# Optimization experiments

Measured on AMD Instinct MI355X. Metric: run time of the kernel, lower is better.

## Reference

```python
import jax, jax.numpy as jnp
import numpy as np

B, C, H, W = 16, 512, 32, 32
NH = 8
HD = C // NH


def setup_inputs() -> dict:
    key = jax.random.key(0)
    k1, k2, k3 = jax.random.split(key, 3)
    x = jax.random.normal(k1, (B, C, H, W), dtype=jnp.float32)
    w_qkv = jax.random.normal(k2, (3 * C, C), dtype=jnp.float32) * (1.0 / np.sqrt(C))
    w_proj = jax.random.normal(k3, (C, C), dtype=jnp.float32) * (1.0 / np.sqrt(C))
    b_proj = jnp.zeros((C,), dtype=jnp.float32)
    return {"x": x, "w_qkv": w_qkv, "w_proj": w_proj, "b_proj": b_proj}


def reference(x, w_qkv, w_proj, b_proj):
    b, c, h, w = x.shape
    n = h * w
    # 1x1 conv qkv: (3C, C) applied per pixel
    qkv = jnp.einsum('oc,bchw->bohw', w_qkv, x)  # [B, 3C, H, W]
    qkv = qkv.reshape(b, 3, NH, HD, n)           # [B, 3, nh, hd, N]
    qkv = jnp.transpose(qkv, (1, 0, 2, 4, 3))    # [3, B, nh, N, hd]
    q, k, v = qkv[0], qkv[1], qkv[2]
    scale = HD ** -0.5
    scores = jnp.einsum('bhnd,bhmd->bhnm', q, k) * scale  # [B, nh, N, N]
    attn = jax.nn.softmax(scores, axis=-1)
    out = jnp.einsum('bhnm,bhmd->bhnd', attn, v)          # [B, nh, N, hd]
    out = jnp.transpose(out, (0, 1, 3, 2)).reshape(b, c, h, w)
    # 1x1 conv proj with bias
    out = jnp.einsum('oc,bchw->bohw', w_proj, out) + b_proj[None, :, None, None]
    return out
```

## Files before the change

### kernel.cpp

```cpp
#include <hip/hip_runtime.h>
#include <hip/hip_bf16.h>
#include <math.h>

#define BB 16
#define CC 512
#define NH 8
#define HD 64
#define NN 1024
#define THREEC 1536

#define QSCALE 0.18033688f

typedef __attribute__((ext_vector_type(8))) short bf16x8;
typedef __attribute__((ext_vector_type(4))) float f32x4;
typedef __attribute__((ext_vector_type(16))) float f32x16;

#if __has_builtin(__builtin_amdgcn_exp2f)
#define EXP2F __builtin_amdgcn_exp2f
#else
#define EXP2F exp2f
#endif

#define XT_OFF 0u
#define WQ_OFF 16777216u
#define WP_OFF 18350080u
#define QB_OFF 18874368u
#define KB_OFF 35651584u
#define VT_OFF 52428800u
#define AB_OFF 69206016u

static __device__ inline unsigned short f2bf(float f) {
  union { float f; unsigned u; } v; v.f = f;
  unsigned r = v.u + 0x7fffu + ((v.u >> 16) & 1u);
  return (unsigned short)(r >> 16);
}

static __device__ inline unsigned pk2bf(float a, float b) {
#if defined(__AMDGCN__) && __has_builtin(__builtin_amdgcn_cvt_pk_bf16_f32)
  typedef __attribute__((ext_vector_type(2))) __bf16 bfp2;
  union { bfp2 v; unsigned u; } z;
  z.v = __builtin_amdgcn_cvt_pk_bf16_f32(a, b);
  return z.u;
#else
  return (unsigned)f2bf(a) | ((unsigned)f2bf(b) << 16);
#endif
}

static __device__ inline void gld_lds16(const unsigned short* g, unsigned short* l) {
  __builtin_amdgcn_global_load_lds(
      (const __attribute__((address_space(1))) unsigned int*)g,
      (__attribute__((address_space(3))) unsigned int*)l, 16, 0, 0);
}

__global__ __launch_bounds__(256) void prep_w(const float* __restrict__ wqkv,
                                              const float* __restrict__ wproj,
                                              unsigned short* __restrict__ dq,
                                              unsigned short* __restrict__ dp) {
  const size_t i8 = ((size_t)blockIdx.x * 256 + threadIdx.x) * 8;
  const float* src;
  unsigned short* dst;
  if (i8 < 786432u) { src = wqkv + i8; dst = dq + i8; }
  else              { src = wproj + (i8 - 786432u); dst = dp + (i8 - 786432u); }
  float4 a = *(const float4*)src;
  float4 b = *(const float4*)(src + 4);
  unsigned short pk[8] = {f2bf(a.x), f2bf(a.y), f2bf(a.z), f2bf(a.w),
                          f2bf(b.x), f2bf(b.y), f2bf(b.z), f2bf(b.w)};
  *(uint4*)dst = *(const uint4*)pk;
}

__global__ __launch_bounds__(256) void prep_xT(const float* __restrict__ x,
                                               unsigned short* __restrict__ xT) {
  const int b  = blockIdx.z;
  const int c0 = blockIdx.y * 64;
  const int n0 = blockIdx.x * 64;
  __shared__ float tile[64][65];
  const int t  = threadIdx.x;
  const int cl = t >> 4, n4 = (t & 15) * 4;
#pragma unroll
  for (int r = 0; r < 4; ++r) {
    float4 v = *(const float4*)&x[((size_t)b * CC + c0 + cl + 16 * r) * NN + n0 + n4];
    *(float4*)&tile[cl + 16 * r][n4] = v;
  }
  __syncthreads();
  const int nl = t >> 4, c4 = (t & 15) * 4;
#pragma unroll
  for (int r = 0; r < 4; ++r) {
    ushort4 p;
    p.x = f2bf(tile[c4 + 0][nl + 16 * r]);
    p.y = f2bf(tile[c4 + 1][nl + 16 * r]);
    p.z = f2bf(tile[c4 + 2][nl + 16 * r]);
    p.w = f2bf(tile[c4 + 3][nl + 16 * r]);
    *(ushort4*)&xT[((size_t)b * NN + n0 + nl + 16 * r) * CC + c0 + c4] = p;
  }
}

__global__ __launch_bounds__(256) void qkv_mfma(const unsigned short* __restrict__ wq,
                                                const unsigned short* __restrict__ xT,
                                                unsigned short* __restrict__ qb,
                                                unsigned short* __restrict__ kb_,
                                                unsigned short* __restrict__ vt) {
  const int b  = blockIdx.z;
  const int o0 = blockIdx.y * 128;
  const int n0 = blockIdx.x * 128;
  const int t  = threadIdx.x;
  const int w    = t >> 6;
  const int lane = t & 63;
  const int quad = lane >> 4;
  const int l16  = lane & 15;
  const int m_off = (w >> 1) * 64;
  const int n_off = (w & 1) * 64;

  __shared__ unsigned short sm[17408];
  unsigned short* As = sm;
  unsigned short* Bs = sm + 8192;

  const int which = o0 >> 9;
  const bool vmode = (which == 2);

  const int srow = lane >> 3;
  const int ssw  = ((lane & 7) ^ srow) * 8;
  const unsigned short* gA = wq + (size_t)(o0 + 32 * w + srow) * CC + ssw;
  const unsigned short* gB = xT + ((size_t)b * NN + n0 + 32 * w + srow) * CC + ssw;

  f32x4 acc[4][4] = {};

  for (int c0 = 0; c0 < CC; c0 += 64) {
    __syncthreads();
#pragma unroll
    for (int L = 0; L < 4; ++L) {
      gld_lds16(gA + (size_t)(8 * L) * CC + c0, &As[(32 * w + 8 * L) * 64]);
      gld_lds16(gB + (size_t)(8 * L) * CC + c0, &Bs[(32 * w + 8 * L) * 64]);
    }
    __syncthreads();
    const unsigned short* Af = vmode ? Bs : As;
    const unsigned short* Bf = vmode ? As : Bs;
#pragma unroll
    for (int ks = 0; ks < 2; ++ks) {
      const int ph = ((ks * 4 + quad) ^ (l16 & 7)) * 8;
      bf16x8 af[4], bfr[4];
#pragma unroll
      for (int i = 0; i < 4; ++i) {
        af[i]  = *(const bf16x8*)&Af[(m_off + 16 * i + l16) * 64 + ph];
        bfr[i] = *(const bf16x8*)&Bf[(n_off + 16 * i + l16) * 64 + ph];
      }
#pragma unroll
      for (int i = 0; i < 4; ++i)
#pragma unroll
        for (int j = 0; j < 4; ++j)
          acc[i][j] = __builtin_amdgcn_mfma_f32_16x16x32_bf16(af[i], bfr[j], acc[i][j], 0, 0, 0);
    }
  }

  __syncthreads();
  const float sc = (which == 0) ? QSCALE : 1.0f;
#pragma unroll
  for (int i = 0; i < 4; ++i) {
#pragma unroll
    for (int j = 0; j < 4; ++j) {
      const int Drow = m_off + 16 * i + quad * 4;
      const int Dcol = n_off + 16 * j + l16;
      ushort4 p;
      p.x = f2bf(acc[i][j][0] * sc);
      p.y = f2bf(acc[i][j][1] * sc);
      p.z = f2bf(acc[i][j][2] * sc);
      p.w = f2bf(acc[i][j][3] * sc);
      *(ushort4*)&sm[Dcol * 136 + Drow] = p;
    }
  }
  __syncthreads();
  const int lrow = t >> 1;
  const int half = t & 1;
  const unsigned short* src = &sm[lrow * 136 + 64 * half];
  if (!vmode) {
    const int hh = ((o0 >> 6) & 7) + half;
    unsigned short* dst = (which == 0 ? qb : kb_) +
        ((size_t)(b * NH + hh) * NN + n0 + lrow) * HD;
#pragma unroll
    for (int i = 0; i < 8; ++i) *(uint4*)(dst + 8 * i) = *(const uint4*)(src + 8 * i);
  } else {
    const int hh = ((o0 + lrow) >> 6) & 7;
    const int d  = lrow & 63;
    unsigned short* dst = vt + ((size_t)(b * NH + hh) * HD + d) * NN + n0 + 64 * half;
#pragma unroll
    for (int i = 0; i < 8; ++i) *(uint4*)(dst + 8 * i) = *(const uint4*)(src + 8 * i);
  }
}

__global__ __launch_bounds__(256) void attn_mfma(const unsigned short* __restrict__ Qg,
                                                 const unsigned short* __restrict__ Kg,
                                                 const unsigned short* __restrict__ Vtg,
                                                 unsigned short* __restrict__ attnB) {
  const int bh = blockIdx.x;
  const int b  = bh >> 3;
  const int h  = bh & 7;
  const int n0 = blockIdx.y * 128;
  const int t  = threadIdx.x;
  const int w    = t >> 6;
  const int lane = t & 63;
  const int l31  = lane & 31;
  const int hi   = lane >> 5;

  __shared__ unsigned short sm[9216];
  unsigned short* Ks = sm;
  unsigned short* Vt = sm + 4096;

  const unsigned short* qrow = Qg + ((size_t)bh * NN + n0 + w * 32 + l31) * HD + hi * 8;
  bf16x8 qf[4];
#pragma unroll
  for (int c = 0; c < 4; ++c) qf[c] = *(const bf16x8*)(qrow + 16 * c);

  const int krow = (l31 & ~12) | ((l31 & 4) << 1) | ((l31 & 8) >> 1);
  const int ksw  = krow & 7;
  const int vsw  = l31 & 7;

  f32x16 oacc[2] = {};
  float lx = 0.f, ly = 0.f;

  const int srow = lane >> 3;
  const int sgrp = (lane & 7) ^ (srow & 7);
  const unsigned short* kstage = Kg + (size_t)bh * NN * HD +
                                 (size_t)(16 * w + srow) * HD + sgrp * 8;
  const unsigned short* vstage = Vtg + (size_t)bh * HD * NN +
                                 (size_t)(16 * w + srow) * NN + sgrp * 8;
  unsigned short* ksl0 = &Ks[(16 * w) * 64];
  unsigned short* ksl1 = &Ks[(16 * w + 8) * 64];
  unsigned short* vsl0 = &Vt[(16 * w) * 64];
  unsigned short* vsl1 = &Vt[(16 * w + 8) * 64];

#pragma unroll 1
  for (int j0 = 0; j0 < NN; j0 += 64) {
    __syncthreads();
    gld_lds16(kstage + (size_t)j0 * HD, ksl0);
    gld_lds16(kstage + (size_t)(j0 + 8) * HD, ksl1);
    gld_lds16(vstage + j0, vsl0);
    gld_lds16(vstage + (size_t)8 * NN + j0, vsl1);
    __syncthreads();

#pragma unroll
    for (int kb = 0; kb < 2; ++kb) {
      f32x16 st = {};
      const unsigned short* krp = &Ks[(32 * kb + krow) * 64];
#pragma unroll
      for (int c = 0; c < 4; ++c) {
        bf16x8 kf = *(const bf16x8*)(krp + (((2 * c + hi) ^ ksw) * 8));
        st = __builtin_amdgcn_mfma_f32_32x32x16_bf16(kf, qf[c], st, 0, 0, 0);
      }
      float e[16];
#pragma unroll
      for (int i = 0; i < 8; ++i) {
        e[2 * i]     = EXP2F(st[2 * i]);
        e[2 * i + 1] = EXP2F(st[2 * i + 1]);
        lx += e[2 * i];
        ly += e[2 * i + 1];
      }
      unsigned P[8];
#pragma unroll
      for (int i = 0; i < 8; ++i) P[i] = pk2bf(e[2 * i], e[2 * i + 1]);

#pragma unroll
      for (int g = 0; g < 2; ++g) {
        union { unsigned u[4]; bf16x8 v; } cv;
        cv.u[0] = P[4 * g + 0]; cv.u[1] = P[4 * g + 1];
        cv.u[2] = P[4 * g + 2]; cv.u[3] = P[4 * g + 3];
#pragma unroll
        for (int mt = 0; mt < 2; ++mt) {
          const int vrow = 32 * mt + l31;
          bf16x8 vf = *(const bf16x8*)&Vt[vrow * 64 + (((4 * kb + 2 * g + hi) ^ vsw) * 8)];
          oacc[mt] = __builtin_amdgcn_mfma_f32_32x32x16_bf16(vf, cv.v, oacc[mt], 0, 0, 0);
        }
      }
    }
  }

  float lsum = lx + ly;
  lsum += __shfl_xor(lsum, 32);
  const float inv = 1.0f / lsum;

  __syncthreads();
  unsigned short* Es = sm + w * 2304;
#pragma unroll
  for (int mt = 0; mt < 2; ++mt) {
#pragma unroll
    for (int rr = 0; rr < 4; ++rr) {
      const int d = 32 * mt + 8 * rr + 4 * hi;
      ushort4 p;
      p.x = f2bf(oacc[mt][4 * rr + 0] * inv);
      p.y = f2bf(oacc[mt][4 * rr + 1] * inv);
      p.z = f2bf(oacc[mt][4 * rr + 2] * inv);
      p.w = f2bf(oacc[mt][4 * rr + 3] * inv);
      *(ushort4*)&Es[l31 * 72 + d] = p;
    }
  }
  const int q    = lane >> 1;
  const int half = lane & 1;
  const unsigned short* src = &Es[q * 72 + 32 * half];
  unsigned short* gdst = attnB + ((size_t)b * NN + n0 + w * 32 + q) * CC + h * HD + 32 * half;
#pragma unroll
  for (int i = 0; i < 4; ++i) *(uint4*)(gdst + 8 * i) = *(const uint4*)(src + 8 * i);
}

__global__ __launch_bounds__(256) void proj_mfma(const unsigned short* __restrict__ wp,
                                                 const unsigned short* __restrict__ aB,
                                                 const float* __restrict__ bias,
                                                 float* __restrict__ out) {
  const int b  = blockIdx.z;
  const int o0 = blockIdx.y * 128;
  const int n0 = blockIdx.x * 128;
  const int t  = threadIdx.x;
  const int w    = t >> 6;
  const int lane = t & 63;
  const int quad = lane >> 4;
  const int l16  = lane & 15;
  const int m_off = (w >> 1) * 64;
  const int n_off = (w & 1) * 64;

  __shared__ unsigned short sm[16384];
  unsigned short* As = sm;
  unsigned short* Bs = sm + 8192;

  const int srow = lane >> 3;
  const int ssw  = ((lane & 7) ^ srow) * 8;
  const unsigned short* gA = wp + (size_t)(o0 + 32 * w + srow) * CC + ssw;
  const unsigned short* gB = aB + ((size_t)b * NN + n0 + 32 * w + srow) * CC + ssw;

  f32x4 acc[4][4] = {};

  for (int c0 = 0; c0 < CC; c0 += 64) {
    __syncthreads();
#pragma unroll
    for (int L = 0; L < 4; ++L) {
      gld_lds16(gA + (size_t)(8 * L) * CC + c0, &As[(32 * w + 8 * L) * 64]);
      gld_lds16(gB + (size_t)(8 * L) * CC + c0, &Bs[(32 * w + 8 * L) * 64]);
    }
    __syncthreads();
#pragma unroll
    for (int ks = 0; ks < 2; ++ks) {
      const int ph = ((ks * 4 + quad) ^ (l16 & 7)) * 8;
      bf16x8 af[4], bfr[4];
#pragma unroll
      for (int i = 0; i < 4; ++i) {
        af[i]  = *(const bf16x8*)&As[(m_off + 16 * i + l16) * 64 + ph];
        bfr[i] = *(const bf16x8*)&Bs[(n_off + 16 * i + l16) * 64 + ph];
      }
#pragma unroll
      for (int i = 0; i < 4; ++i)
#pragma unroll
        for (int j = 0; j < 4; ++j)
          acc[i][j] = __builtin_amdgcn_mfma_f32_16x16x32_bf16(af[i], bfr[j], acc[i][j], 0, 0, 0);
    }
  }

#pragma unroll
  for (int i = 0; i < 4; ++i) {
#pragma unroll
    for (int r = 0; r < 4; ++r) {
      const int o = o0 + m_off + 16 * i + quad * 4 + r;
      const float bv = bias[o];
      float* orow = out + ((size_t)b * CC + o) * NN + n0 + n_off;
#pragma unroll
      for (int j = 0; j < 4; ++j)
        orow[16 * j + l16] = acc[i][j][r] + bv;
    }
  }
}

extern "C" void kernel_launch(void* const* d_in, const int* in_sizes, int n_in,
                              void* d_out, int out_size, void* d_ws, size_t ws_size,
                              hipStream_t stream) {
  const float* x      = (const float*)d_in[0];
  const float* w_qkv  = (const float*)d_in[1];
  const float* w_proj = (const float*)d_in[2];
  const float* b_proj = (const float*)d_in[3];
  char* wsb  = (char*)d_ws;
  float* out = (float*)d_out;

  unsigned short* xT  = (unsigned short*)(wsb + XT_OFF);
  unsigned short* wq  = (unsigned short*)(wsb + WQ_OFF);
  unsigned short* wp  = (unsigned short*)(wsb + WP_OFF);
  unsigned short* qb  = (unsigned short*)(wsb + QB_OFF);
  unsigned short* kb_ = (unsigned short*)(wsb + KB_OFF);
  unsigned short* vt  = (unsigned short*)(wsb + VT_OFF);
  unsigned short* aB  = (unsigned short*)(wsb + AB_OFF);

  prep_w<<<512, 256, 0, stream>>>(w_qkv, w_proj, wq, wp);
  prep_xT<<<dim3(16, 8, BB), 256, 0, stream>>>(x, xT);
  qkv_mfma<<<dim3(8, 12, BB), 256, 0, stream>>>(wq, xT, qb, kb_, vt);
  attn_mfma<<<dim3(BB * NH, NN / 128), 256, 0, stream>>>(qb, kb_, vt, aB);
  proj_mfma<<<dim3(8, 4, BB), 256, 0, stream>>>(wp, aB, b_proj, out);
}
```

Measured before the change: 199.1 us.

## Double-buffer K/V tiles in LDS and raise wave priority around MFMA

The attention kernel now keeps two LDS buffers for the K and V tiles. It prefetches the next 64-key tile into the idle buffer while computing on the current one, so each iteration needs one barrier instead of two. This is meant to hide global-to-LDS load latency behind the QK and PV MFMA work. It also brackets the MFMA sequences with s_setprio so matrix issue is favoured over other waves. The cost is LDS per block growing from about 18 KB to 32 KB, which may lower occupancy, and the scheme relies on the barrier waiting for the asynchronous LDS loads.

New measurement: 201.3 us. About the same (+1.1%).

```diff
diff --git a/kernel.cpp b/kernel.cpp
--- a/kernel.cpp
+++ b/kernel.cpp
@@ -200,9 +200,7 @@
   const int l31  = lane & 31;
   const int hi   = lane >> 5;
 
-  __shared__ unsigned short sm[9216];
-  unsigned short* Ks = sm;
-  unsigned short* Vt = sm + 4096;
+  __shared__ unsigned short sm[16384];
 
   const unsigned short* qrow = Qg + ((size_t)bh * NN + n0 + w * 32 + l31) * HD + hi * 8;
   bf16x8 qf[4];
@@ -222,29 +220,40 @@
                                  (size_t)(16 * w + srow) * HD + sgrp * 8;
   const unsigned short* vstage = Vtg + (size_t)bh * HD * NN +
                                  (size_t)(16 * w + srow) * NN + sgrp * 8;
-  unsigned short* ksl0 = &Ks[(16 * w) * 64];
-  unsigned short* ksl1 = &Ks[(16 * w + 8) * 64];
-  unsigned short* vsl0 = &Vt[(16 * w) * 64];
-  unsigned short* vsl1 = &Vt[(16 * w + 8) * 64];
+  const int kso0 = (16 * w) * 64;
+  const int kso1 = (16 * w + 8) * 64;
+
+  auto stage = [&](int j0, int p) {
+    unsigned short* Kp = sm + p * 8192;
+    unsigned short* Vp = Kp + 4096;
+    gld_lds16(kstage + (size_t)j0 * HD, Kp + kso0);
+    gld_lds16(kstage + (size_t)(j0 + 8) * HD, Kp + kso1);
+    gld_lds16(vstage + j0, Vp + kso0);
+    gld_lds16(vstage + (size_t)8 * NN + j0, Vp + kso1);
+  };
+
+  stage(0, 0);
+  int cur = 0;
 
 #pragma unroll 1
   for (int j0 = 0; j0 < NN; j0 += 64) {
     __syncthreads();
-    gld_lds16(kstage + (size_t)j0 * HD, ksl0);
-    gld_lds16(kstage + (size_t)(j0 + 8) * HD, ksl1);
-    gld_lds16(vstage + j0, vsl0);
-    gld_lds16(vstage + (size_t)8 * NN + j0, vsl1);
-    __syncthreads();
+    if (j0 + 64 < NN) stage(j0 + 64, cur ^ 1);
+
+    const unsigned short* Ks = sm + cur * 8192;
+    const unsigned short* Vt = Ks + 4096;
 
 #pragma unroll
     for (int kb = 0; kb < 2; ++kb) {
       f32x16 st = {};
       const unsigned short* krp = &Ks[(32 * kb + krow) * 64];
+      __builtin_amdgcn_s_setprio(1);
 #pragma unroll
       for (int c = 0; c < 4; ++c) {
         bf16x8 kf = *(const bf16x8*)(krp + (((2 * c + hi) ^ ksw) * 8));
         st = __builtin_amdgcn_mfma_f32_32x32x16_bf16(kf, qf[c], st, 0, 0, 0);
       }
+      __builtin_amdgcn_s_setprio(0);
       float e[16];
 #pragma unroll
       for (int i = 0; i < 8; ++i) {
@@ -257,6 +266,7 @@
 #pragma unroll
       for (int i = 0; i < 8; ++i) P[i] = pk2bf(e[2 * i], e[2 * i + 1]);
 
+      __builtin_amdgcn_s_setprio(1);
 #pragma unroll
       for (int g = 0; g < 2; ++g) {
         union { unsigned u[4]; bf16x8 v; } cv;
@@ -269,7 +279,9 @@
           oacc[mt] = __builtin_amdgcn_mfma_f32_32x32x16_bf16(vf, cv.v, oacc[mt], 0, 0, 0);
         }
       }
-    }
+      __builtin_amdgcn_s_setprio(0);
+    }
+    cur ^= 1;
   }
 
   float lsum = lx + ly;
```

## Load K/V fragments directly from global into registers with double buffering

Applied to the files above, without the earlier changes.

The attention kernel no longer stages K and V tiles through shared memory with block-wide barriers. Each wave now loads its own K and V^T fragments straight from global memory into registers, double-buffered across 32-key steps, and raises wave priority around the MFMA sections. A launch bound of 4 blocks per CU is added to limit register use. This removes the LDS staging and the per-tile syncs, but every wave now re-reads K/V from global/L2 (four times the traffic per block) with uncoalesced 16-byte row accesses, and register pressure rises.

Measured after the change: 269.5 us. 35.3% more time.

```diff
diff --git a/kernel.cpp b/kernel.cpp
--- a/kernel.cpp
+++ b/kernel.cpp
@@ -186,10 +186,10 @@
   }
 }
 
-__global__ __launch_bounds__(256) void attn_mfma(const unsigned short* __restrict__ Qg,
-                                                 const unsigned short* __restrict__ Kg,
-                                                 const unsigned short* __restrict__ Vtg,
-                                                 unsigned short* __restrict__ attnB) {
+__global__ __launch_bounds__(256, 4) void attn_mfma(const unsigned short* __restrict__ Qg,
+                                                    const unsigned short* __restrict__ Kg,
+                                                    const unsigned short* __restrict__ Vtg,
+                                                    unsigned short* __restrict__ attnB) {
   const int bh = blockIdx.x;
   const int b  = bh >> 3;
   const int h  = bh & 7;
@@ -201,8 +201,6 @@
   const int hi   = lane >> 5;
 
   __shared__ unsigned short sm[9216];
-  unsigned short* Ks = sm;
-  unsigned short* Vt = sm + 4096;
 
   const unsigned short* qrow = Qg + ((size_t)bh * NN + n0 + w * 32 + l31) * HD + hi * 8;
   bf16x8 qf[4];
@@ -210,73 +208,86 @@
   for (int c = 0; c < 4; ++c) qf[c] = *(const bf16x8*)(qrow + 16 * c);
 
   const int krow = (l31 & ~12) | ((l31 & 4) << 1) | ((l31 & 8) >> 1);
-  const int ksw  = krow & 7;
-  const int vsw  = l31 & 7;
-
+
+  const unsigned short* Kl = Kg + ((size_t)bh * NN + krow) * HD + 8 * hi;
+  const unsigned short* Vl = Vtg + ((size_t)bh * HD + l31) * NN + 8 * hi;
+
+  const f32x16 fz = {};
   f32x16 oacc[2] = {};
   float lx = 0.f, ly = 0.f;
 
-  const int srow = lane >> 3;
-  const int sgrp = (lane & 7) ^ (srow & 7);
-  const unsigned short* kstage = Kg + (size_t)bh * NN * HD +
-                                 (size_t)(16 * w + srow) * HD + sgrp * 8;
-  const unsigned short* vstage = Vtg + (size_t)bh * HD * NN +
-                                 (size_t)(16 * w + srow) * NN + sgrp * 8;
-  unsigned short* ksl0 = &Ks[(16 * w) * 64];
-  unsigned short* ksl1 = &Ks[(16 * w + 8) * 64];
-  unsigned short* vsl0 = &Vt[(16 * w) * 64];
-  unsigned short* vsl1 = &Vt[(16 * w + 8) * 64];
-
+  auto LDK = [&](bf16x8* kf, int s) {
+    const unsigned short* p = Kl + (size_t)s * 32 * HD;
+#pragma unroll
+    for (int c = 0; c < 4; ++c) kf[c] = *(const bf16x8*)(p + 16 * c);
+  };
+  auto LDV = [&](bf16x8* vf, int s) {
+    const unsigned short* p = Vl + 32 * s;
+#pragma unroll
+    for (int g = 0; g < 2; ++g)
+#pragma unroll
+      for (int mt = 0; mt < 2; ++mt)
+        vf[2 * g + mt] = *(const bf16x8*)(p + (size_t)mt * 32 * NN + 16 * g);
+  };
+  auto QK = [&](const bf16x8* kf) -> f32x16 {
+    f32x16 st = __builtin_amdgcn_mfma_f32_32x32x16_bf16(kf[0], qf[0], fz, 0, 0, 0);
+#pragma unroll
+    for (int c = 1; c < 4; ++c)
+      st = __builtin_amdgcn_mfma_f32_32x32x16_bf16(kf[c], qf[c], st, 0, 0, 0);
+    return st;
+  };
+  auto SM = [&](const f32x16& st, unsigned* P) {
+#pragma unroll
+    for (int i = 0; i < 8; ++i) {
+      float ea = EXP2F(st[2 * i]);
+      float eb = EXP2F(st[2 * i + 1]);
+      lx += ea; ly += eb;
+      P[i] = pk2bf(ea, eb);
+    }
+  };
+  auto PV = [&](const bf16x8* vf, const unsigned* P) {
+#pragma unroll
+    for (int g = 0; g < 2; ++g) {
+      union { unsigned u[4]; bf16x8 v; } cv;
+      cv.u[0] = P[4 * g + 0]; cv.u[1] = P[4 * g + 1];
+      cv.u[2] = P[4 * g + 2]; cv.u[3] = P[4 * g + 3];
+#pragma unroll
+      for (int mt = 0; mt < 2; ++mt)
+        oacc[mt] = __builtin_amdgcn_mfma_f32_32x32x16_bf16(vf[2 * g + mt], cv.v, oacc[mt], 0, 0, 0);
+    }
+  };
+
+  bf16x8 kA[4], kB[4], vA[4], vB[4];
+  unsigned P[8];
+
+  LDK(kA, 0);
 #pragma unroll 1
-  for (int j0 = 0; j0 < NN; j0 += 64) {
-    __syncthreads();
-    gld_lds16(kstage + (size_t)j0 * HD, ksl0);
-    gld_lds16(kstage + (size_t)(j0 + 8) * HD, ksl1);
-    gld_lds16(vstage + j0, vsl0);
-    gld_lds16(vstage + (size_t)8 * NN + j0, vsl1);
-    __syncthreads();
-
-#pragma unroll
-    for (int kb = 0; kb < 2; ++kb) {
-      f32x16 st = {};
-      const unsigned short* krp = &Ks[(32 * kb + krow) * 64];
-#pragma unroll
-      for (int c = 0; c < 4; ++c) {
-        bf16x8 kf = *(const bf16x8*)(krp + (((2 * c + hi) ^ ksw) * 8));
-        st = __builtin_amdgcn_mfma_f32_32x32x16_bf16(kf, qf[c], st, 0, 0, 0);
-      }
-      float e[16];
-#pragma unroll
-      for (int i = 0; i < 8; ++i) {
-        e[2 * i]     = EXP2F(st[2 * i]);
-        e[2 * i + 1] = EXP2F(st[2 * i + 1]);
-        lx += e[2 * i];
-        ly += e[2 * i + 1];
-      }
-      unsigned P[8];
-#pragma unroll
-      for (int i = 0; i < 8; ++i) P[i] = pk2bf(e[2 * i], e[2 * i + 1]);
-
-#pragma unroll
-      for (int g = 0; g < 2; ++g) {
-        union { unsigned u[4]; bf16x8 v; } cv;
-        cv.u[0] = P[4 * g + 0]; cv.u[1] = P[4 * g + 1];
-        cv.u[2] = P[4 * g + 2]; cv.u[3] = P[4 * g + 3];
-#pragma unroll
-        for (int mt = 0; mt < 2; ++mt) {
-          const int vrow = 32 * mt + l31;
-          bf16x8 vf = *(const bf16x8*)&Vt[vrow * 64 + (((4 * kb + 2 * g + hi) ^ vsw) * 8)];
-          oacc[mt] = __builtin_amdgcn_mfma_f32_32x32x16_bf16(vf, cv.v, oacc[mt], 0, 0, 0);
-        }
-      }
-    }
+  for (int s = 0; s < 32; s += 2) {
+    LDK(kB, s + 1);
+    LDV(vA, s);
+    __builtin_amdgcn_s_setprio(1);
+    f32x16 st = QK(kA);
+    __builtin_amdgcn_s_setprio(0);
+    SM(st, P);
+    __builtin_amdgcn_s_setprio(1);
+    PV(vA, P);
+    __builtin_amdgcn_s_setprio(0);
+
+    if (s + 2 < 32) LDK(kA, s + 2);
+    LDV(vB, s + 1);
+    __builtin_amdgcn_s_setprio(1);
+    f32x16 st2 = QK(kB);
+    __builtin_amdgcn_s_setprio(0);
+    SM(st2, P);
+    __builtin_amdgcn_s_setprio(1);
+    PV(vB, P);
+    __builtin_amdgcn_s_setprio(0);
   }
 
   float lsum = lx + ly;
   lsum += __shfl_xor(lsum, 32);
   const float inv = 1.0f / lsum;
 
-  __syncthreads();
   unsigned short* Es = sm + w * 2304;
 #pragma unroll
   for (int mt = 0; mt < 2; ++mt) {
```
